# Performance work log

Hardware: AMD Instinct MI355X
Metric: run time of the kernel (lower is better)

Reference implementation:

```python
import jax, jax.numpy as jnp
import numpy as np

EPS = 1e-7  # tf.keras.backend.epsilon()
ROUTING = 3
C, L = 32, 32

def squash(s):
    # 'Dynamic routing between capsules' squash: (|s|^2/(1+|s|^2)) * s/|s|
    n = jnp.linalg.norm(s, axis=-1, keepdims=True)
    return (n ** 2 / (1 + n ** 2) / (n + EPS)) * s

def setup_inputs() -> dict:
    key = jax.random.key(0)
    k1, k2 = jax.random.split(key)
    B, H, Wd, iC, iL = 32, 8, 8, 32, 32
    inputs = jax.random.normal(k1, (B, H, Wd, iC, iL), dtype=jnp.float32)
    N = H * Wd * iC  # 2048 input capsules
    # glorot_uniform for W: [N, input_L, C*L]
    limit = float(np.sqrt(6.0 / (iL + C * L)))
    W = jax.random.uniform(k2, (N, iL, C * L), minval=-limit, maxval=limit, dtype=jnp.float32)
    biases = jnp.zeros((C, L), dtype=jnp.float32)  # 'zeros' initializer
    return {"inputs": inputs, "W": W, "biases": biases}

def reference(inputs, W, biases):
    B = inputs.shape[0]
    N, iL = W.shape[0], W.shape[1]
    x = inputs.reshape(B, N, iL)
    # per-capsule prediction: u[b,j,k] = sum_i x[b,j,i] * W[j,i,k]
    u = jnp.einsum('bji,jik->bjk', x, W).reshape(B, N, C, L)
    b = jnp.zeros((B, N, C, 1), dtype=u.dtype)
    v = jnp.zeros((B, C, L), dtype=u.dtype)
    for r in range(ROUTING):
        c = jax.nn.softmax(b, axis=2)                 # coupling coeffs over C
        s = jnp.sum(u * c, axis=1) + biases           # [B,C,L]
        # NOTE: CapsuleAttentionBlock applied here in original (source not
        # provided in this module); treated as identity.
        v = squash(s)                                 # [B,C,L]
        if r < ROUTING - 1:
            b = b + jnp.sum(u * v[:, None, :, :], axis=-1, keepdims=True)
    return v
```

## Files before the change

kernel.cpp:

```cpp
#include <hip/hip_runtime.h>
#include <hip/hip_bf16.h>

#define NB    32
#define NCAP  2048
#define CL    1024
#define ILEN  32

__device__ inline unsigned int pack2_bf16(float lo, float hi) {
    unsigned int a = __float_as_uint(lo);
    a += 0x7FFFu + ((a >> 16) & 1u);
    unsigned int b = __float_as_uint(hi);
    b += 0x7FFFu + ((b >> 16) & 1u);
    return (a >> 16) | (b & 0xFFFF0000u);
}

__device__ inline void unpack8(uint4 a, float* f) {
    f[0] = __uint_as_float(a.x << 16);
    f[1] = __uint_as_float(a.x & 0xFFFF0000u);
    f[2] = __uint_as_float(a.y << 16);
    f[3] = __uint_as_float(a.y & 0xFFFF0000u);
    f[4] = __uint_as_float(a.z << 16);
    f[5] = __uint_as_float(a.z & 0xFFFF0000u);
    f[6] = __uint_as_float(a.w << 16);
    f[7] = __uint_as_float(a.w & 0xFFFF0000u);
}

__global__ __launch_bounds__(256) void compute_u(const float* __restrict__ x,
                                                 const float* __restrict__ W,
                                                 unsigned short* __restrict__ u) {
    const int j    = blockIdx.x >> 1;
    const int kh   = blockIdx.x & 1;
    const int t    = threadIdx.x;
    const int wv   = t >> 6;
    const int lane = t & 63;

    __shared__ float xs[32][32];

    {
        int b  = t & 31;
        int i4 = (t >> 5) << 2;
        float4 v = *(const float4*)(x + ((size_t)b * NCAP + j) * ILEN + i4);
        xs[i4 + 0][b] = v.x;
        xs[i4 + 1][b] = v.y;
        xs[i4 + 2][b] = v.z;
        xs[i4 + 3][b] = v.w;
    }
    __syncthreads();

    const float* Wb = W + (size_t)j * (ILEN * CL) + kh * 512 + lane * 8;

    float acc[8][8];
#pragma unroll
    for (int bb = 0; bb < 8; ++bb)
#pragma unroll
        for (int kk = 0; kk < 8; ++kk) acc[bb][kk] = 0.f;

#pragma unroll 4
    for (int i = 0; i < 32; ++i) {
        float4 w0 = *(const float4*)(Wb + (size_t)i * CL);
        float4 w1 = *(const float4*)(Wb + (size_t)i * CL + 4);
        float4 x0 = *(const float4*)(&xs[i][wv * 8]);
        float4 x1 = *(const float4*)(&xs[i][wv * 8 + 4]);
        float wk[8] = {w0.x, w0.y, w0.z, w0.w, w1.x, w1.y, w1.z, w1.w};
        float xv[8] = {x0.x, x0.y, x0.z, x0.w, x1.x, x1.y, x1.z, x1.w};
#pragma unroll
        for (int bb = 0; bb < 8; ++bb)
#pragma unroll
            for (int kk = 0; kk < 8; ++kk)
                acc[bb][kk] += xv[bb] * wk[kk];
    }

    const int k = kh * 512 + lane * 8;
#pragma unroll
    for (int bb = 0; bb < 8; ++bb) {
        int b = wv * 8 + bb;
        uint4 o;
        o.x = pack2_bf16(acc[bb][0], acc[bb][1]);
        o.y = pack2_bf16(acc[bb][2], acc[bb][3]);
        o.z = pack2_bf16(acc[bb][4], acc[bb][5]);
        o.w = pack2_bf16(acc[bb][6], acc[bb][7]);
        *(uint4*)(u + ((size_t)b * NCAP + j) * CL + k) = o;
    }
}

template<bool HAS_V>
__global__ __launch_bounds__(256) void route_pass(const unsigned short* __restrict__ u,
                                                  const float* __restrict__ vlog,
                                                  float* __restrict__ spart) {
    const int b    = blockIdx.x;
    const int jc   = blockIdx.y;
    const int t    = threadIdx.x;
    const int wv   = t >> 6;
    const int lane = t & 63;
    const int c0   = lane >> 2;
    const int sub  = lane & 3;
    const int e0   = c0 * 32 + sub * 8;

    float vme0[8], vme1[8];
    if (HAS_V) {
        const float* vb = vlog + b * CL;
        *(float4*)(vme0)     = *(const float4*)(vb + e0);
        *(float4*)(vme0 + 4) = *(const float4*)(vb + e0 + 4);
        *(float4*)(vme1)     = *(const float4*)(vb + e0 + 512);
        *(float4*)(vme1 + 4) = *(const float4*)(vb + e0 + 516);
    }

    const int jbase = jc * 128 + wv * 32;
    const unsigned short* up = u + ((size_t)b * NCAP + jbase) * CL + e0;

    float acc0[8], acc1[8];
#pragma unroll
    for (int e = 0; e < 8; ++e) { acc0[e] = 0.f; acc1[e] = 0.f; }

    uint4 ca0 = *(const uint4*)(up + 0 * CL);
    uint4 cg0 = *(const uint4*)(up + 0 * CL + 512);
    uint4 ca1 = *(const uint4*)(up + 1 * CL);
    uint4 cg1 = *(const uint4*)(up + 1 * CL + 512);
    uint4 pa0 = *(const uint4*)(up + 2 * CL);
    uint4 pg0 = *(const uint4*)(up + 2 * CL + 512);
    uint4 pa1 = *(const uint4*)(up + 3 * CL);
    uint4 pg1 = *(const uint4*)(up + 3 * CL + 512);

    for (int jj = 0; jj < 32; jj += 2) {
        const int j4 = (jj + 4 < 32) ? jj + 4 : 31;
        const int j5 = (jj + 5 < 32) ? jj + 5 : 31;
        uint4 na0 = *(const uint4*)(up + (size_t)j4 * CL);
        uint4 ng0 = *(const uint4*)(up + (size_t)j4 * CL + 512);
        uint4 na1 = *(const uint4*)(up + (size_t)j5 * CL);
        uint4 ng1 = *(const uint4*)(up + (size_t)j5 * CL + 512);

        float uf0[8], uf1[8], uf2[8], uf3[8];
        unpack8(ca0, uf0); unpack8(cg0, uf1);
        unpack8(ca1, uf2); unpack8(cg1, uf3);

        float cw0, cw1, cw2, cw3;
        if (HAS_V) {
            float p0 = 0.f, p1 = 0.f, p2 = 0.f, p3 = 0.f;
#pragma unroll
            for (int e = 0; e < 8; ++e) {
                p0 += uf0[e] * vme0[e];
                p1 += uf1[e] * vme1[e];
                p2 += uf2[e] * vme0[e];
                p3 += uf3[e] * vme1[e];
            }
            p0 += __shfl_xor(p0, 1); p0 += __shfl_xor(p0, 2);
            p1 += __shfl_xor(p1, 1); p1 += __shfl_xor(p1, 2);
            p2 += __shfl_xor(p2, 1); p2 += __shfl_xor(p2, 2);
            p3 += __shfl_xor(p3, 1); p3 += __shfl_xor(p3, 2);
            float m0 = fmaxf(p0, p1);
            float m1 = fmaxf(p2, p3);
            m0 = fmaxf(m0, __shfl_xor(m0, 4));
            m1 = fmaxf(m1, __shfl_xor(m1, 4));
            m0 = fmaxf(m0, __shfl_xor(m0, 8));
            m1 = fmaxf(m1, __shfl_xor(m1, 8));
            m0 = fmaxf(m0, __shfl_xor(m0, 16));
            m1 = fmaxf(m1, __shfl_xor(m1, 16));
            m0 = fmaxf(m0, __shfl_xor(m0, 32));
            m1 = fmaxf(m1, __shfl_xor(m1, 32));
            float e00 = __expf(p0 - m0), e01 = __expf(p1 - m0);
            float e10 = __expf(p2 - m1), e11 = __expf(p3 - m1);
            float s0 = e00 + e01, s1 = e10 + e11;
            s0 += __shfl_xor(s0, 4);
            s1 += __shfl_xor(s1, 4);
            s0 += __shfl_xor(s0, 8);
            s1 += __shfl_xor(s1, 8);
            s0 += __shfl_xor(s0, 16);
            s1 += __shfl_xor(s1, 16);
            s0 += __shfl_xor(s0, 32);
            s1 += __shfl_xor(s1, 32);
            float i0 = __builtin_amdgcn_rcpf(s0);
            float i1 = __builtin_amdgcn_rcpf(s1);
            cw0 = e00 * i0; cw1 = e01 * i0;
            cw2 = e10 * i1; cw3 = e11 * i1;
        } else {
            cw0 = cw1 = cw2 = cw3 = 0.03125f;
        }
#pragma unroll
        for (int e = 0; e < 8; ++e) {
            acc0[e] += cw0 * uf0[e] + cw2 * uf2[e];
            acc1[e] += cw1 * uf1[e] + cw3 * uf3[e];
        }
        ca0 = pa0; cg0 = pg0; ca1 = pa1; cg1 = pg1;
        pa0 = na0; pg0 = ng0; pa1 = na1; pg1 = ng1;
    }

    __shared__ float red[4][1024];
    *(float4*)(&red[wv][e0])       = *(float4*)(acc0);
    *(float4*)(&red[wv][e0 + 4])   = *(float4*)(acc0 + 4);
    *(float4*)(&red[wv][e0 + 512]) = *(float4*)(acc1);
    *(float4*)(&red[wv][e0 + 516]) = *(float4*)(acc1 + 4);
    __syncthreads();

    const int o = t * 4;
    float4 r0 = *(float4*)(&red[0][o]);
    float4 r1 = *(float4*)(&red[1][o]);
    float4 r2 = *(float4*)(&red[2][o]);
    float4 r3 = *(float4*)(&red[3][o]);
    float4 r;
    r.x = (r0.x + r1.x) + (r2.x + r3.x);
    r.y = (r0.y + r1.y) + (r2.y + r3.y);
    r.z = (r0.z + r1.z) + (r2.z + r3.z);
    r.w = (r0.w + r1.w) + (r2.w + r3.w);
    *(float4*)(spart + ((size_t)b * 16 + jc) * CL + o) = r;
}

__global__ __launch_bounds__(256) void squash_kernel(const float* __restrict__ spart,
                                                     const float* __restrict__ biases,
                                                     float* __restrict__ vout,
                                                     float* __restrict__ vlog_out,
                                                     const float* __restrict__ vprev) {
    const int b = blockIdx.x;
    const int t = threadIdx.x;

    float4 sv = make_float4(0.f, 0.f, 0.f, 0.f);
#pragma unroll
    for (int p = 0; p < 16; ++p) {
        float4 q = *(const float4*)(spart + ((size_t)b * 16 + p) * CL + t * 4);
        sv.x += q.x; sv.y += q.y; sv.z += q.z; sv.w += q.w;
    }
    float4 bi = *(const float4*)(biases + t * 4);
    sv.x += bi.x; sv.y += bi.y; sv.z += bi.z; sv.w += bi.w;

    float n2 = sv.x * sv.x + sv.y * sv.y + sv.z * sv.z + sv.w * sv.w;
    n2 += __shfl_xor(n2, 1);
    n2 += __shfl_xor(n2, 2);
    n2 += __shfl_xor(n2, 4);

    float n = sqrtf(n2);
    float f = n2 / ((1.f + n2) * (n + 1e-7f));

    float4 v;
    v.x = f * sv.x; v.y = f * sv.y; v.z = f * sv.z; v.w = f * sv.w;
    *(float4*)(vout + b * CL + t * 4) = v;

    if (vlog_out != nullptr) {
        float4 a = make_float4(0.f, 0.f, 0.f, 0.f);
        if (vprev != nullptr) a = *(const float4*)(vprev + b * CL + t * 4);
        float4 o;
        o.x = v.x + a.x; o.y = v.y + a.y; o.z = v.z + a.z; o.w = v.w + a.w;
        *(float4*)(vlog_out + b * CL + t * 4) = o;
    }
}

extern "C" void kernel_launch(void* const* d_in, const int* in_sizes, int n_in,
                              void* d_out, int out_size, void* d_ws, size_t ws_size,
                              hipStream_t stream) {
    const float* x      = (const float*)d_in[0];
    const float* W      = (const float*)d_in[1];
    const float* biases = (const float*)d_in[2];
    float* out = (float*)d_out;

    unsigned short* u = (unsigned short*)d_ws;
    float* fb    = (float*)((char*)d_ws + (size_t)NB * NCAP * CL * 2);
    float* spart = fb;
    float* v0    = spart + 524288;
    float* vl2   = v0 + 32768;
    float* vdmp  = vl2 + 32768;

    compute_u<<<NCAP * 2, 256, 0, stream>>>(x, W, u);

    dim3 rg(NB, 16);
    route_pass<false><<<rg, 256, 0, stream>>>(u, nullptr, spart);
    squash_kernel<<<NB, 256, 0, stream>>>(spart, biases, v0, nullptr, nullptr);
    route_pass<true><<<rg, 256, 0, stream>>>(u, v0, spart);
    squash_kernel<<<NB, 256, 0, stream>>>(spart, biases, vdmp, vl2, v0);
    route_pass<true><<<rg, 256, 0, stream>>>(u, vl2, spart);
    squash_kernel<<<NB, 256, 0, stream>>>(spart, biases, out, nullptr, nullptr);
}
```

Baseline: 479.1 us.

## Fuse uniform first routing pass into u computation and squash into route kernels

The first routing iteration uses uniform coupling of 1/32, so its per-capsule sums are now accumulated in fp32 while u is computed, with each block handling 8 capsules. This removes one full read of the bf16 u tensor. The later routing passes accumulate into s with float atomics, and a last-block counter lets the final block of each batch apply squash and add the logits, which drops the separate squash launches. In exchange, compute_u runs with 8x fewer blocks, which reduces parallelism for streaming W. It also writes an extra 32MB partial-sum buffer, and the atomics make the summation order nondeterministic.

```diff
diff --git a/kernel.cpp b/kernel.cpp
--- a/kernel.cpp
+++ b/kernel.cpp
@@ -25,68 +25,133 @@
     f[7] = __uint_as_float(a.w & 0xFFFF0000u);
 }
 
-__global__ __launch_bounds__(256) void compute_u(const float* __restrict__ x,
-                                                 const float* __restrict__ W,
-                                                 unsigned short* __restrict__ u) {
-    const int j    = blockIdx.x >> 1;
+__global__ __launch_bounds__(256) void compute_u_fused(const float* __restrict__ x,
+                                                       const float* __restrict__ W,
+                                                       unsigned short* __restrict__ u,
+                                                       float* __restrict__ spart0) {
+    const int jc   = blockIdx.x >> 1;
     const int kh   = blockIdx.x & 1;
     const int t    = threadIdx.x;
     const int wv   = t >> 6;
     const int lane = t & 63;
 
-    __shared__ float xs[32][32];
+    __shared__ float xs[8][32][32];
 
     {
-        int b  = t & 31;
-        int i4 = (t >> 5) << 2;
-        float4 v = *(const float4*)(x + ((size_t)b * NCAP + j) * ILEN + i4);
-        xs[i4 + 0][b] = v.x;
-        xs[i4 + 1][b] = v.y;
-        xs[i4 + 2][b] = v.z;
-        xs[i4 + 3][b] = v.w;
+        const int b0  = t & 31;
+        const int i40 = (t >> 5) << 2;
+#pragma unroll
+        for (int jj = 0; jj < 8; ++jj) {
+            float4 v = *(const float4*)(x + ((size_t)b0 * NCAP + (size_t)(jc * 8 + jj)) * ILEN + i40);
+            xs[jj][i40 + 0][b0] = v.x;
+            xs[jj][i40 + 1][b0] = v.y;
+            xs[jj][i40 + 2][b0] = v.z;
+            xs[jj][i40 + 3][b0] = v.w;
+        }
     }
     __syncthreads();
 
-    const float* Wb = W + (size_t)j * (ILEN * CL) + kh * 512 + lane * 8;
-
-    float acc[8][8];
+    const int k = kh * 512 + lane * 8;
+
+    float s0[8][8];
 #pragma unroll
     for (int bb = 0; bb < 8; ++bb)
 #pragma unroll
-        for (int kk = 0; kk < 8; ++kk) acc[bb][kk] = 0.f;
+        for (int kk = 0; kk < 8; ++kk) s0[bb][kk] = 0.f;
+
+    for (int jj = 0; jj < 8; ++jj) {
+        const int j = jc * 8 + jj;
+        const float* Wb = W + (size_t)j * (ILEN * CL) + k;
+
+        float acc[8][8];
+#pragma unroll
+        for (int bb = 0; bb < 8; ++bb)
+#pragma unroll
+            for (int kk = 0; kk < 8; ++kk) acc[bb][kk] = 0.f;
 
 #pragma unroll 4
-    for (int i = 0; i < 32; ++i) {
-        float4 w0 = *(const float4*)(Wb + (size_t)i * CL);
-        float4 w1 = *(const float4*)(Wb + (size_t)i * CL + 4);
-        float4 x0 = *(const float4*)(&xs[i][wv * 8]);
-        float4 x1 = *(const float4*)(&xs[i][wv * 8 + 4]);
-        float wk[8] = {w0.x, w0.y, w0.z, w0.w, w1.x, w1.y, w1.z, w1.w};
-        float xv[8] = {x0.x, x0.y, x0.z, x0.w, x1.x, x1.y, x1.z, x1.w};
-#pragma unroll
-        for (int bb = 0; bb < 8; ++bb)
-#pragma unroll
-            for (int kk = 0; kk < 8; ++kk)
-                acc[bb][kk] += xv[bb] * wk[kk];
-    }
-
-    const int k = kh * 512 + lane * 8;
+        for (int i = 0; i < 32; ++i) {
+            float4 w0 = *(const float4*)(Wb + (size_t)i * CL);
+            float4 w1 = *(const float4*)(Wb + (size_t)i * CL + 4);
+            float4 x0 = *(const float4*)(&xs[jj][i][wv * 8]);
+            float4 x1 = *(const float4*)(&xs[jj][i][wv * 8 + 4]);
+            float wk[8] = {w0.x, w0.y, w0.z, w0.w, w1.x, w1.y, w1.z, w1.w};
+            float xv[8] = {x0.x, x0.y, x0.z, x0.w, x1.x, x1.y, x1.z, x1.w};
+#pragma unroll
+            for (int bb = 0; bb < 8; ++bb)
+#pragma unroll
+                for (int kk = 0; kk < 8; ++kk)
+                    acc[bb][kk] += xv[bb] * wk[kk];
+        }
+
+#pragma unroll
+        for (int bb = 0; bb < 8; ++bb) {
+            int b = wv * 8 + bb;
+            uint4 o;
+            o.x = pack2_bf16(acc[bb][0], acc[bb][1]);
+            o.y = pack2_bf16(acc[bb][2], acc[bb][3]);
+            o.z = pack2_bf16(acc[bb][4], acc[bb][5]);
+            o.w = pack2_bf16(acc[bb][6], acc[bb][7]);
+            *(uint4*)(u + ((size_t)b * NCAP + j) * CL + k) = o;
+#pragma unroll
+            for (int kk = 0; kk < 8; ++kk) s0[bb][kk] += acc[bb][kk];
+        }
+    }
+
 #pragma unroll
     for (int bb = 0; bb < 8; ++bb) {
         int b = wv * 8 + bb;
-        uint4 o;
-        o.x = pack2_bf16(acc[bb][0], acc[bb][1]);
-        o.y = pack2_bf16(acc[bb][2], acc[bb][3]);
-        o.z = pack2_bf16(acc[bb][4], acc[bb][5]);
-        o.w = pack2_bf16(acc[bb][6], acc[bb][7]);
-        *(uint4*)(u + ((size_t)b * NCAP + j) * CL + k) = o;
-    }
-}
-
-template<bool HAS_V>
-__global__ __launch_bounds__(256) void route_pass(const unsigned short* __restrict__ u,
-                                                  const float* __restrict__ vlog,
-                                                  float* __restrict__ spart) {
+        float* sp = spart0 + ((size_t)jc * 32 + b) * CL + k;
+        *(float4*)(sp)     = *(float4*)(&s0[bb][0]);
+        *(float4*)(sp + 4) = *(float4*)(&s0[bb][4]);
+    }
+}
+
+__global__ __launch_bounds__(256) void squash0(const float* __restrict__ spart0,
+                                               const float* __restrict__ biases,
+                                               float* __restrict__ v0,
+                                               float* __restrict__ s1,
+                                               float* __restrict__ s2,
+                                               int* __restrict__ cnt) {
+    const int b = blockIdx.x;
+    const int t = threadIdx.x;
+    const int o = t * 4;
+
+    *(float4*)(s1 + b * CL + o) = make_float4(0.f, 0.f, 0.f, 0.f);
+    *(float4*)(s2 + b * CL + o) = make_float4(0.f, 0.f, 0.f, 0.f);
+    if (b == 0 && t < 64) cnt[t] = 0;
+
+    float4 sv = make_float4(0.f, 0.f, 0.f, 0.f);
+    for (int p = 0; p < 256; ++p) {
+        float4 q = *(const float4*)(spart0 + ((size_t)p * 32 + b) * CL + o);
+        sv.x += q.x; sv.y += q.y; sv.z += q.z; sv.w += q.w;
+    }
+    float4 bi = *(const float4*)(biases + o);
+    const float inv32 = 1.f / 32.f;
+    sv.x = sv.x * inv32 + bi.x;
+    sv.y = sv.y * inv32 + bi.y;
+    sv.z = sv.z * inv32 + bi.z;
+    sv.w = sv.w * inv32 + bi.w;
+
+    float n2 = sv.x * sv.x + sv.y * sv.y + sv.z * sv.z + sv.w * sv.w;
+    n2 += __shfl_xor(n2, 1);
+    n2 += __shfl_xor(n2, 2);
+    n2 += __shfl_xor(n2, 4);
+    float n = sqrtf(n2);
+    float f = n2 / ((1.f + n2) * (n + 1e-7f));
+
+    float4 v;
+    v.x = f * sv.x; v.y = f * sv.y; v.z = f * sv.z; v.w = f * sv.w;
+    *(float4*)(v0 + b * CL + o) = v;
+}
+
+__global__ __launch_bounds__(256) void route_fused(const unsigned short* __restrict__ u,
+                                                   const float* __restrict__ vin,
+                                                   float* __restrict__ sbuf,
+                                                   int* __restrict__ cnt,
+                                                   const float* __restrict__ biases,
+                                                   const float* __restrict__ vadd,
+                                                   float* __restrict__ vout) {
     const int b    = blockIdx.x;
     const int jc   = blockIdx.y;
     const int t    = threadIdx.x;
@@ -97,8 +162,8 @@
     const int e0   = c0 * 32 + sub * 8;
 
     float vme0[8], vme1[8];
-    if (HAS_V) {
-        const float* vb = vlog + b * CL;
+    {
+        const float* vb = vin + b * CL;
         *(float4*)(vme0)     = *(const float4*)(vb + e0);
         *(float4*)(vme0 + 4) = *(const float4*)(vb + e0 + 4);
         *(float4*)(vme1)     = *(const float4*)(vb + e0 + 512);
@@ -133,48 +198,43 @@
         unpack8(ca0, uf0); unpack8(cg0, uf1);
         unpack8(ca1, uf2); unpack8(cg1, uf3);
 
-        float cw0, cw1, cw2, cw3;
-        if (HAS_V) {
-            float p0 = 0.f, p1 = 0.f, p2 = 0.f, p3 = 0.f;
-#pragma unroll
-            for (int e = 0; e < 8; ++e) {
-                p0 += uf0[e] * vme0[e];
-                p1 += uf1[e] * vme1[e];
-                p2 += uf2[e] * vme0[e];
-                p3 += uf3[e] * vme1[e];
-            }
-            p0 += __shfl_xor(p0, 1); p0 += __shfl_xor(p0, 2);
-            p1 += __shfl_xor(p1, 1); p1 += __shfl_xor(p1, 2);
-            p2 += __shfl_xor(p2, 1); p2 += __shfl_xor(p2, 2);
-            p3 += __shfl_xor(p3, 1); p3 += __shfl_xor(p3, 2);
-            float m0 = fmaxf(p0, p1);
-            float m1 = fmaxf(p2, p3);
-            m0 = fmaxf(m0, __shfl_xor(m0, 4));
-            m1 = fmaxf(m1, __shfl_xor(m1, 4));
-            m0 = fmaxf(m0, __shfl_xor(m0, 8));
-            m1 = fmaxf(m1, __shfl_xor(m1, 8));
-            m0 = fmaxf(m0, __shfl_xor(m0, 16));
-            m1 = fmaxf(m1, __shfl_xor(m1, 16));
-            m0 = fmaxf(m0, __shfl_xor(m0, 32));
-            m1 = fmaxf(m1, __shfl_xor(m1, 32));
-            float e00 = __expf(p0 - m0), e01 = __expf(p1 - m0);
-            float e10 = __expf(p2 - m1), e11 = __expf(p3 - m1);
-            float s0 = e00 + e01, s1 = e10 + e11;
-            s0 += __shfl_xor(s0, 4);
-            s1 += __shfl_xor(s1, 4);
-            s0 += __shfl_xor(s0, 8);
-            s1 += __shfl_xor(s1, 8);
-            s0 += __shfl_xor(s0, 16);
-            s1 += __shfl_xor(s1, 16);
-            s0 += __shfl_xor(s0, 32);
-            s1 += __shfl_xor(s1, 32);
-            float i0 = __builtin_amdgcn_rcpf(s0);
-            float i1 = __builtin_amdgcn_rcpf(s1);
-            cw0 = e00 * i0; cw1 = e01 * i0;
-            cw2 = e10 * i1; cw3 = e11 * i1;
-        } else {
-            cw0 = cw1 = cw2 = cw3 = 0.03125f;
-        }
+        float p0 = 0.f, p1 = 0.f, p2 = 0.f, p3 = 0.f;
+#pragma unroll
+        for (int e = 0; e < 8; ++e) {
+            p0 += uf0[e] * vme0[e];
+            p1 += uf1[e] * vme1[e];
+            p2 += uf2[e] * vme0[e];
+            p3 += uf3[e] * vme1[e];
+        }
+        p0 += __shfl_xor(p0, 1); p0 += __shfl_xor(p0, 2);
+        p1 += __shfl_xor(p1, 1); p1 += __shfl_xor(p1, 2);
+        p2 += __shfl_xor(p2, 1); p2 += __shfl_xor(p2, 2);
+        p3 += __shfl_xor(p3, 1); p3 += __shfl_xor(p3, 2);
+        float m0 = fmaxf(p0, p1);
+        float m1 = fmaxf(p2, p3);
+        m0 = fmaxf(m0, __shfl_xor(m0, 4));
+        m1 = fmaxf(m1, __shfl_xor(m1, 4));
+        m0 = fmaxf(m0, __shfl_xor(m0, 8));
+        m1 = fmaxf(m1, __shfl_xor(m1, 8));
+        m0 = fmaxf(m0, __shfl_xor(m0, 16));
+        m1 = fmaxf(m1, __shfl_xor(m1, 16));
+        m0 = fmaxf(m0, __shfl_xor(m0, 32));
+        m1 = fmaxf(m1, __shfl_xor(m1, 32));
+        float e00 = __expf(p0 - m0), e01 = __expf(p1 - m0);
+        float e10 = __expf(p2 - m1), e11 = __expf(p3 - m1);
+        float s0 = e00 + e01, s1 = e10 + e11;
+        s0 += __shfl_xor(s0, 4);
+        s1 += __shfl_xor(s1, 4);
+        s0 += __shfl_xor(s0, 8);
+        s1 += __shfl_xor(s1, 8);
+        s0 += __shfl_xor(s0, 16);
+        s1 += __shfl_xor(s1, 16);
+        s0 += __shfl_xor(s0, 32);
+        s1 += __shfl_xor(s1, 32);
+        float i0 = __builtin_amdgcn_rcpf(s0);
+        float i1 = __builtin_amdgcn_rcpf(s1);
+        float cw0 = e00 * i0, cw1 = e01 * i0;
+        float cw2 = e10 * i1, cw3 = e11 * i1;
 #pragma unroll
         for (int e = 0; e < 8; ++e) {
             acc0[e] += cw0 * uf0[e] + cw2 * uf2[e];
@@ -192,54 +252,47 @@
     __syncthreads();
 
     const int o = t * 4;
-    float4 r0 = *(float4*)(&red[0][o]);
-    float4 r1 = *(float4*)(&red[1][o]);
-    float4 r2 = *(float4*)(&red[2][o]);
-    float4 r3 = *(float4*)(&red[3][o]);
-    float4 r;
-    r.x = (r0.x + r1.x) + (r2.x + r3.x);
-    r.y = (r0.y + r1.y) + (r2.y + r3.y);
-    r.z = (r0.z + r1.z) + (r2.z + r3.z);
-    r.w = (r0.w + r1.w) + (r2.w + r3.w);
-    *(float4*)(spart + ((size_t)b * 16 + jc) * CL + o) = r;
-}
-
-__global__ __launch_bounds__(256) void squash_kernel(const float* __restrict__ spart,
-                                                     const float* __restrict__ biases,
-                                                     float* __restrict__ vout,
-                                                     float* __restrict__ vlog_out,
-                                                     const float* __restrict__ vprev) {
-    const int b = blockIdx.x;
-    const int t = threadIdx.x;
-
-    float4 sv = make_float4(0.f, 0.f, 0.f, 0.f);
-#pragma unroll
-    for (int p = 0; p < 16; ++p) {
-        float4 q = *(const float4*)(spart + ((size_t)b * 16 + p) * CL + t * 4);
-        sv.x += q.x; sv.y += q.y; sv.z += q.z; sv.w += q.w;
-    }
-    float4 bi = *(const float4*)(biases + t * 4);
+    float* sb = sbuf + b * CL;
+    {
+        float4 r0 = *(float4*)(&red[0][o]);
+        float4 r1 = *(float4*)(&red[1][o]);
+        float4 r2 = *(float4*)(&red[2][o]);
+        float4 r3 = *(float4*)(&red[3][o]);
+        atomicAdd(sb + o + 0, (r0.x + r1.x) + (r2.x + r3.x));
+        atomicAdd(sb + o + 1, (r0.y + r1.y) + (r2.y + r3.y));
+        atomicAdd(sb + o + 2, (r0.z + r1.z) + (r2.z + r3.z));
+        atomicAdd(sb + o + 3, (r0.w + r1.w) + (r2.w + r3.w));
+    }
+
+    __threadfence();
+    __syncthreads();
+    __shared__ int last;
+    if (t == 0) last = (atomicAdd(&cnt[b], 1) == 15) ? 1 : 0;
+    __syncthreads();
+    if (!last) return;
+
+    float4 sv;
+    sv.x = atomicAdd(sb + o + 0, 0.f);
+    sv.y = atomicAdd(sb + o + 1, 0.f);
+    sv.z = atomicAdd(sb + o + 2, 0.f);
+    sv.w = atomicAdd(sb + o + 3, 0.f);
+    float4 bi = *(const float4*)(biases + o);
     sv.x += bi.x; sv.y += bi.y; sv.z += bi.z; sv.w += bi.w;
 
     float n2 = sv.x * sv.x + sv.y * sv.y + sv.z * sv.z + sv.w * sv.w;
     n2 += __shfl_xor(n2, 1);
     n2 += __shfl_xor(n2, 2);
     n2 += __shfl_xor(n2, 4);
-
     float n = sqrtf(n2);
     float f = n2 / ((1.f + n2) * (n + 1e-7f));
 
     float4 v;
     v.x = f * sv.x; v.y = f * sv.y; v.z = f * sv.z; v.w = f * sv.w;
-    *(float4*)(vout + b * CL + t * 4) = v;
-
-    if (vlog_out != nullptr) {
-        float4 a = make_float4(0.f, 0.f, 0.f, 0.f);
-        if (vprev != nullptr) a = *(const float4*)(vprev + b * CL + t * 4);
-        float4 o;
-        o.x = v.x + a.x; o.y = v.y + a.y; o.z = v.z + a.z; o.w = v.w + a.w;
-        *(float4*)(vlog_out + b * CL + t * 4) = o;
-    }
+    if (vadd != nullptr) {
+        float4 a = *(const float4*)(vadd + b * CL + o);
+        v.x += a.x; v.y += a.y; v.z += a.z; v.w += a.w;
+    }
+    *(float4*)(vout + b * CL + o) = v;
 }
 
 extern "C" void kernel_launch(void* const* d_in, const int* in_sizes, int n_in,
@@ -251,19 +304,17 @@
     float* out = (float*)d_out;
 
     unsigned short* u = (unsigned short*)d_ws;
-    float* fb    = (float*)((char*)d_ws + (size_t)NB * NCAP * CL * 2);
-    float* spart = fb;
-    float* v0    = spart + 524288;
-    float* vl2   = v0 + 32768;
-    float* vdmp  = vl2 + 32768;
-
-    compute_u<<<NCAP * 2, 256, 0, stream>>>(x, W, u);
-
+    float* fb     = (float*)((char*)d_ws + (size_t)NB * NCAP * CL * 2);
+    float* spart0 = fb;
+    float* s1     = spart0 + 256 * 32 * CL;
+    float* s2     = s1 + NB * CL;
+    float* v0     = s2 + NB * CL;
+    float* vl2    = v0 + NB * CL;
+    int*   cnt    = (int*)(vl2 + NB * CL);
+
+    compute_u_fused<<<512, 256, 0, stream>>>(x, W, u, spart0);
+    squash0<<<NB, 256, 0, stream>>>(spart0, biases, v0, s1, s2, cnt);
     dim3 rg(NB, 16);
-    route_pass<false><<<rg, 256, 0, stream>>>(u, nullptr, spart);
-    squash_kernel<<<NB, 256, 0, stream>>>(spart, biases, v0, nullptr, nullptr);
-    route_pass<true><<<rg, 256, 0, stream>>>(u, v0, spart);
-    squash_kernel<<<NB, 256, 0, stream>>>(spart, biases, vdmp, vl2, v0);
-    route_pass<true><<<rg, 256, 0, stream>>>(u, vl2, spart);
-    squash_kernel<<<NB, 256, 0, stream>>>(spart, biases, out, nullptr, nullptr);
-}
+    route_fused<<<rg, 256, 0, stream>>>(u, v0, s1, cnt, biases, v0, vl2);
+    route_fused<<<rg, 256, 0, stream>>>(u, vl2, s2, cnt + 32, biases, nullptr, out);
+}
```

After: 664.6 us. 38.7% more time.
